# Kernel optimization log

Measured on AMD Instinct MI355X. Metric: run time of the kernel, lower is better.

The kernel has to match this reference:

```python
import jax, jax.numpy as jnp
import numpy as np

# Steady-state MemoryBank contrastive loss (post-warmup, all banks full).
B, D = 1024, 128            # batch, feature_dim
C, K = 50, 4096             # num_classes, per-class bank capacity (memory_size // num_classes)
TEMP = 0.3
TAIL_CLASSES = (0, 1)
TAIL_WEIGHT = 1.3
EPS = 1e-12                 # F.normalize eps


def setup_inputs() -> dict:
    key = jax.random.key(0)
    k1, k2, k3 = jax.random.split(key, 3)
    features = jax.random.normal(k1, (B, D), dtype=jnp.float32)
    labels = jax.random.randint(k2, (B,), 0, C)
    # memory_bank_c buffers, stacked: [C, K, D] (registered as randn in __init__)
    memory = jax.random.normal(k3, (C, K, D), dtype=jnp.float32)
    return {"features": features, "labels": labels, "memory": memory}


def reference(features, labels, memory):
    # L2-normalize features (F.normalize with eps clamp)
    norm = jnp.maximum(jnp.linalg.norm(features, axis=1, keepdims=True), EPS)
    feat = features / norm                                   # [B, D]

    # Similarities of every sample to every bank row, scaled by temperature.
    sims = jnp.einsum('bd,ckd->bck', feat, memory) / TEMP    # [B, C, K]

    # Cross-entropy with target index 0 over concat([pos_bank, neg_banks]):
    # target logit is the first row of the positive (label) bank; the
    # normalizer is logsumexp over ALL bank rows (order-invariant).
    pos_logit = sims[jnp.arange(B), labels, 0]               # [B]
    lse = jax.nn.logsumexp(sims.reshape(B, C * K), axis=1)   # [B]
    per_sample = lse - pos_logit                             # -log softmax[0]

    tail = jnp.isin(labels, jnp.asarray(TAIL_CLASSES))
    weights = jnp.where(tail, TAIL_WEIGHT, 1.0)
    # All B samples are valid in steady state -> divide by B.
    return jnp.sum(weights * per_sample) / B
```

## Files before the change

### kernel.cpp

```cpp
#include <hip/hip_runtime.h>


#define XCHUNK 128
#define NITER 25
#define TILE_BYTES 32768
#define LN2f 0.6931471805599453f
#define SCALEf 4.808983469629878f

typedef __attribute__((ext_vector_type(8))) short bf16x8;
typedef __attribute__((ext_vector_type(4))) float f32x4;
typedef unsigned int u32;

__device__ __forceinline__ unsigned short f2bf(float x) {
    union { float f; unsigned int u; } c; c.f = x;
    unsigned int u = c.u;
    u = (u + 0x7fffu + ((u >> 16) & 1u)) >> 16;
    return (unsigned short)u;
}
__device__ __forceinline__ float bf2f(unsigned short h) {
    union { unsigned int u; float f; } c; c.u = ((unsigned int)h) << 16;
    return c.f;
}
__device__ __forceinline__ unsigned int pack_bf2(float lo, float hi) {
    union { float f; unsigned int u; } a, b; a.f = lo; b.f = hi;
    return __builtin_amdgcn_perm(b.u, a.u, 0x07060302u);
}
__device__ __forceinline__ void gl_lds16(const void* gp, void* lp) {
    __builtin_amdgcn_global_load_lds(
        (const __attribute__((address_space(1))) u32*)gp,
        (__attribute__((address_space(3))) u32*)lp, 16, 0, 0);
}

__global__ void normalize_feat(const float* __restrict__ f,
                               unsigned short* __restrict__ featb,
                               float* __restrict__ S,
                               float* __restrict__ out) {
    const int b = blockIdx.x;
    const int t = threadIdx.x;
    if (t == 0) S[b] = 0.0f;
    if (b == 0 && t == 1) *out = 0.0f;
    float v = f[b * 128 + t];
    float ss = v * v;
    #pragma unroll
    for (int m = 1; m < 64; m <<= 1) ss += __shfl_xor(ss, m, 64);
    __shared__ float wsum[2];
    if ((t & 63) == 0) wsum[t >> 6] = ss;
    __syncthreads();
    float tot = wsum[0] + wsum[1];
    float inv = SCALEf / fmaxf(sqrtf(tot), 1e-12f);
    featb[b * 128 + t] = f2bf(v * inv);
}

__global__ __launch_bounds__(256, 2) void gemm_lse(
        const unsigned short* __restrict__ featb,
        const float* __restrict__ mem,
        float* __restrict__ S)
{
    __shared__ float ldsb[2][64 * 128];

    const int tid  = threadIdx.x;
    const int wave = tid >> 6;
    const int lane = tid & 63;
    const int col  = lane & 15;
    const int quad = lane >> 4;
    const int c3   = col & 7;

    const int m_wave = blockIdx.y * 256 + wave * 64;
    const int xc = blockIdx.x;

    bf16x8 afrag[4][4];
    #pragma unroll
    for (int mf = 0; mf < 4; ++mf)
        #pragma unroll
        for (int ks = 0; ks < 4; ++ks)
            afrag[mf][ks] = *(const bf16x8*)&featb[(size_t)(m_wave + mf * 16 + col) * 128
                                                   + ks * 32 + quad * 8];

    float s_part[16];
    #pragma unroll
    for (int i = 0; i < 16; ++i) s_part[i] = 0.0f;

    int goffb[8];
    #pragma unroll
    for (int i = 0; i < 8; ++i) {
        int s_lin = i * 256 + tid;
        int row  = s_lin >> 5;
        int slot = s_lin & 31;
        int q    = slot ^ (row & 7);
        goffb[i] = row * 512 + q * 16;
    }

    #define STAGE(bi, t_) {                                                     \
        const char* gt = (const char*)mem + (size_t)(xc + XCHUNK * (t_)) * TILE_BYTES; \
        _Pragma("unroll")                                                       \
        for (int i = 0; i < 8; ++i)                                             \
            gl_lds16(gt + goffb[i],                                             \
                     (char*)&ldsb[bi][0] + (i * 4096 + wave * 1024)); }

    #define COMPUTE(bi) {                                                       \
        const float* buf = &ldsb[bi][0];                                        \
        _Pragma("unroll")                                                       \
        for (int nf = 0; nf < 4; ++nf) {                                        \
            const float* rbase = buf + (nf * 16 + col) * 128;                   \
            bf16x8 bfrag[4];                                                    \
            _Pragma("unroll")                                                   \
            for (int ks = 0; ks < 4; ++ks) {                                    \
                int s0 = (((ks * 8 + quad * 2 + 0) ^ c3) * 4);                  \
                int s1 = (((ks * 8 + quad * 2 + 1) ^ c3) * 4);                  \
                float4 f0 = *(const float4*)(rbase + s0);                       \
                float4 f1 = *(const float4*)(rbase + s1);                       \
                uint4 pk;                                                       \
                pk.x = pack_bf2(f0.x, f0.y); pk.y = pack_bf2(f0.z, f0.w);       \
                pk.z = pack_bf2(f1.x, f1.y); pk.w = pack_bf2(f1.z, f1.w);       \
                bfrag[ks] = *(bf16x8*)&pk;                                      \
            }                                                                   \
            f32x4 acc[4];                                                       \
            _Pragma("unroll")                                                   \
            for (int mf = 0; mf < 4; ++mf) acc[mf] = (f32x4)(0.0f);             \
            _Pragma("unroll")                                                   \
            for (int ks = 0; ks < 4; ++ks)                                      \
                _Pragma("unroll")                                               \
                for (int mf = 0; mf < 4; ++mf)                                  \
                    acc[mf] = __builtin_amdgcn_mfma_f32_16x16x32_bf16(          \
                        afrag[mf][ks], bfrag[ks], acc[mf], 0, 0, 0);            \
            _Pragma("unroll")                                                   \
            for (int mf = 0; mf < 4; ++mf)                                      \
                _Pragma("unroll")                                               \
                for (int r = 0; r < 4; ++r)                                     \
                    s_part[mf * 4 + r] += __builtin_amdgcn_exp2f(acc[mf][r]);   \
        } }

    STAGE(0, 0)
    __syncthreads();

    for (int t = 0; t < NITER; ++t) {
        if (t + 1 < NITER) STAGE((t + 1) & 1, t + 1)
        COMPUTE(t & 1)
        __syncthreads();
    }

    #pragma unroll
    for (int d = 1; d < 16; d <<= 1)
        #pragma unroll
        for (int i = 0; i < 16; ++i)
            s_part[i] += __shfl_xor(s_part[i], d, 64);

    if (col == 0) {
        #pragma unroll
        for (int i = 0; i < 16; ++i) {
            int row = m_wave + (i >> 2) * 16 + quad * 4 + (i & 3);
            atomicAdd(&S[row], s_part[i]);
        }
    }
    #undef STAGE
    #undef COMPUTE
}

__global__ void finalize_k(const unsigned short* __restrict__ featb,
                           const float* __restrict__ mem,
                           const int* __restrict__ labels,
                           const float* __restrict__ S,
                           float* __restrict__ out) {
    const int wave = threadIdx.x >> 6;
    const int lane = threadIdx.x & 63;
    const int b = blockIdx.x * 4 + wave;
    const int lab = labels[b];
    const float* mrow = mem + (size_t)lab * (4096 * 128);
    float fa = bf2f(featb[b * 128 + lane]);
    float fc = bf2f(featb[b * 128 + lane + 64]);
    float p = fa * mrow[lane] + fc * mrow[lane + 64];
    #pragma unroll
    for (int m = 1; m < 64; m <<= 1) p += __shfl_xor(p, m, 64);
    if (lane == 0) {
        float w = (lab < 2) ? 1.3f : 1.0f;
        float v = w * LN2f * (log2f(S[b]) - p) * (1.0f / 1024.0f);
        atomicAdd(out, v);
    }
}

extern "C" void kernel_launch(void* const* d_in, const int* in_sizes, int n_in,
                              void* d_out, int out_size, void* d_ws, size_t ws_size,
                              hipStream_t stream) {
    const float* features = (const float*)d_in[0];
    const int*   labels   = (const int*)d_in[1];
    const float* memory   = (const float*)d_in[2];
    float* out = (float*)d_out;

    unsigned short* featb = (unsigned short*)d_ws;
    float* S = (float*)((char*)d_ws + 1024 * 128 * 2);

    normalize_feat<<<1024, 128, 0, stream>>>(features, featb, S, out);
    gemm_lse<<<dim3(XCHUNK, 4), 256, 0, stream>>>(featb, memory, S);
    finalize_k<<<256, 256, 0, stream>>>(featb, memory, labels, S, out);
}
```

Measured before the change: 215.9 us.

## Convert memory tiles to bf16 once at staging and store MFMA-ready fragments in LDS

Global loads of each memory-bank tile now go through registers instead of direct global-to-LDS copies. Each value is converted to bf16 once and written to LDS in the exact per-lane MFMA B-fragment order, so the compute loop reads one 16-byte fragment per k-step with no swizzle or per-wave repacking. Blocks grow to 512 threads covering 512 rows, and the grid changes to 640x2 with 5 iterations, so memory rows are read by half as many blocks. The cost is register-staged prefetch, conversion work on the load path, and a shallower loop per block.

```diff
diff --git a/kernel.cpp b/kernel.cpp
--- a/kernel.cpp
+++ b/kernel.cpp
@@ -1,8 +1,8 @@
 #include <hip/hip_runtime.h>
 
 
-#define XCHUNK 128
-#define NITER 25
+#define XCHUNK 640
+#define NITER 5
 #define TILE_BYTES 32768
 #define LN2f 0.6931471805599453f
 #define SCALEf 4.808983469629878f
@@ -25,11 +25,6 @@
     union { float f; unsigned int u; } a, b; a.f = lo; b.f = hi;
     return __builtin_amdgcn_perm(b.u, a.u, 0x07060302u);
 }
-__device__ __forceinline__ void gl_lds16(const void* gp, void* lp) {
-    __builtin_amdgcn_global_load_lds(
-        (const __attribute__((address_space(1))) u32*)gp,
-        (__attribute__((address_space(3))) u32*)lp, 16, 0, 0);
-}
 
 __global__ void normalize_feat(const float* __restrict__ f,
                                unsigned short* __restrict__ featb,
@@ -51,21 +46,20 @@
     featb[b * 128 + t] = f2bf(v * inv);
 }
 
-__global__ __launch_bounds__(256, 2) void gemm_lse(
+__global__ __launch_bounds__(512, 2) void gemm_lse(
         const unsigned short* __restrict__ featb,
         const float* __restrict__ mem,
         float* __restrict__ S)
 {
-    __shared__ float ldsb[2][64 * 128];
+    __shared__ uint4 ldsb[2][1024];
 
     const int tid  = threadIdx.x;
     const int wave = tid >> 6;
     const int lane = tid & 63;
     const int col  = lane & 15;
     const int quad = lane >> 4;
-    const int c3   = col & 7;
 
-    const int m_wave = blockIdx.y * 256 + wave * 64;
+    const int m_wave = blockIdx.y * 512 + wave * 64;
     const int xc = blockIdx.x;
 
     bf16x8 afrag[4][4];
@@ -80,49 +74,47 @@
     #pragma unroll
     for (int i = 0; i < 16; ++i) s_part[i] = 0.0f;
 
-    int goffb[8];
+    int o[2];
     #pragma unroll
-    for (int i = 0; i < 8; ++i) {
-        int s_lin = i * 256 + tid;
-        int row  = s_lin >> 5;
-        int slot = s_lin & 31;
-        int q    = slot ^ (row & 7);
-        goffb[i] = row * 512 + q * 16;
+    for (int j = 0; j < 2; ++j) {
+        int Sl = j * 512 + tid;
+        int Fi = Sl >> 6, L = Sl & 63;
+        int snf = Fi >> 2, sks = Fi & 3, sq = L >> 4, sc = L & 15;
+        o[j] = (snf * 16 + sc) * 512 + sks * 128 + sq * 32;
     }
 
-    #define STAGE(bi, t_) {                                                     \
+    float4 g0a, g0b, g1a, g1b;
+
+    #define LOADS(t_) {                                                         \
         const char* gt = (const char*)mem + (size_t)(xc + XCHUNK * (t_)) * TILE_BYTES; \
-        _Pragma("unroll")                                                       \
-        for (int i = 0; i < 8; ++i)                                             \
-            gl_lds16(gt + goffb[i],                                             \
-                     (char*)&ldsb[bi][0] + (i * 4096 + wave * 1024)); }
+        g0a = *(const float4*)(gt + o[0]);                                      \
+        g0b = *(const float4*)(gt + o[0] + 16);                                 \
+        g1a = *(const float4*)(gt + o[1]);                                      \
+        g1b = *(const float4*)(gt + o[1] + 16); }
+
+    #define PACKWRITE(bi) {                                                     \
+        uint4 pk;                                                               \
+        pk.x = pack_bf2(g0a.x, g0a.y); pk.y = pack_bf2(g0a.z, g0a.w);           \
+        pk.z = pack_bf2(g0b.x, g0b.y); pk.w = pack_bf2(g0b.z, g0b.w);           \
+        ldsb[bi][tid] = pk;                                                     \
+        pk.x = pack_bf2(g1a.x, g1a.y); pk.y = pack_bf2(g1a.z, g1a.w);           \
+        pk.z = pack_bf2(g1b.x, g1b.y); pk.w = pack_bf2(g1b.z, g1b.w);           \
+        ldsb[bi][512 + tid] = pk; }
 
     #define COMPUTE(bi) {                                                       \
-        const float* buf = &ldsb[bi][0];                                        \
         _Pragma("unroll")                                                       \
         for (int nf = 0; nf < 4; ++nf) {                                        \
-            const float* rbase = buf + (nf * 16 + col) * 128;                   \
-            bf16x8 bfrag[4];                                                    \
-            _Pragma("unroll")                                                   \
-            for (int ks = 0; ks < 4; ++ks) {                                    \
-                int s0 = (((ks * 8 + quad * 2 + 0) ^ c3) * 4);                  \
-                int s1 = (((ks * 8 + quad * 2 + 1) ^ c3) * 4);                  \
-                float4 f0 = *(const float4*)(rbase + s0);                       \
-                float4 f1 = *(const float4*)(rbase + s1);                       \
-                uint4 pk;                                                       \
-                pk.x = pack_bf2(f0.x, f0.y); pk.y = pack_bf2(f0.z, f0.w);       \
-                pk.z = pack_bf2(f1.x, f1.y); pk.w = pack_bf2(f1.z, f1.w);       \
-                bfrag[ks] = *(bf16x8*)&pk;                                      \
-            }                                                                   \
             f32x4 acc[4];                                                       \
             _Pragma("unroll")                                                   \
             for (int mf = 0; mf < 4; ++mf) acc[mf] = (f32x4)(0.0f);             \
             _Pragma("unroll")                                                   \
-            for (int ks = 0; ks < 4; ++ks)                                      \
+            for (int ks = 0; ks < 4; ++ks) {                                    \
+                bf16x8 bfrag = *(const bf16x8*)&ldsb[bi][(nf * 4 + ks) * 64 + lane]; \
                 _Pragma("unroll")                                               \
                 for (int mf = 0; mf < 4; ++mf)                                  \
                     acc[mf] = __builtin_amdgcn_mfma_f32_16x16x32_bf16(          \
-                        afrag[mf][ks], bfrag[ks], acc[mf], 0, 0, 0);            \
+                        afrag[mf][ks], bfrag, acc[mf], 0, 0, 0);                \
+            }                                                                   \
             _Pragma("unroll")                                                   \
             for (int mf = 0; mf < 4; ++mf)                                      \
                 _Pragma("unroll")                                               \
@@ -130,12 +122,14 @@
                     s_part[mf * 4 + r] += __builtin_amdgcn_exp2f(acc[mf][r]);   \
         } }
 
-    STAGE(0, 0)
+    LOADS(0)
+    PACKWRITE(0)
     __syncthreads();
 
     for (int t = 0; t < NITER; ++t) {
-        if (t + 1 < NITER) STAGE((t + 1) & 1, t + 1)
+        if (t + 1 < NITER) LOADS(t + 1)
         COMPUTE(t & 1)
+        if (t + 1 < NITER) PACKWRITE((t + 1) & 1)
         __syncthreads();
     }
 
@@ -152,7 +146,8 @@
             atomicAdd(&S[row], s_part[i]);
         }
     }
-    #undef STAGE
+    #undef LOADS
+    #undef PACKWRITE
     #undef COMPUTE
 }
 
@@ -190,6 +185,6 @@
     float* S = (float*)((char*)d_ws + 1024 * 128 * 2);
 
     normalize_feat<<<1024, 128, 0, stream>>>(features, featb, S, out);
-    gemm_lse<<<dim3(XCHUNK, 4), 256, 0, stream>>>(featb, memory, S);
+    gemm_lse<<<dim3(XCHUNK, 2), 512, 0, stream>>>(featb, memory, S);
     finalize_k<<<256, 256, 0, stream>>>(featb, memory, labels, S, out);
 }
```

Measured after the change: 291.6 us. 1.35x slower.
